# Kernel tuning notes

Hardware: AMD Instinct MI355X
Metric: run time of the kernel (lower is better)

Reference implementation:

```python
import jax, jax.numpy as jnp
import numpy as np

B, K, D, H = 16384, 3, 1024, 16
DH = D // H  # head_dim = 64


def setup_inputs() -> dict:
    key = jax.random.key(0)
    ks = jax.random.split(key, 12)
    s = 1.0 / np.sqrt(D)
    inp = {
        "tokens": jax.random.normal(ks[0], (B, K, D), dtype=jnp.float32),
        "ctx": jax.random.normal(ks[1], (B, 1, D), dtype=jnp.float32),
        "Wq": jax.random.uniform(ks[2], (D, D), jnp.float32, -s, s),
        "bq": jnp.zeros((D,), jnp.float32),
        "Wk": jax.random.uniform(ks[3], (D, D), jnp.float32, -s, s),
        "bk": jnp.zeros((D,), jnp.float32),
        "Wv": jax.random.uniform(ks[4], (D, D), jnp.float32, -s, s),
        "bv": jnp.zeros((D,), jnp.float32),
        "Wc": jax.random.uniform(ks[5], (D, D), jnp.float32, -s, s),
        "bc": jnp.zeros((D,), jnp.float32),
        "Wo": jax.random.uniform(ks[6], (D, D), jnp.float32, -s, s),
        "bo": jnp.zeros((D,), jnp.float32),
    }
    return inp


def _split_heads(x):
    # (B, L, D) -> (B, H, L, DH)
    Bq, L, _ = x.shape
    return x.reshape(Bq, L, H, DH).transpose(0, 2, 1, 3)


def reference(tokens, ctx, Wq, bq, Wk, bk, Wv, bv, Wc, bc, Wo, bo):
    q = _split_heads(tokens @ Wq.T + bq)          # (B,H,K,DH)
    k = _split_heads(tokens @ Wk.T + bk)          # (B,H,K,DH)
    v = _split_heads(tokens @ Wv.T + bv)          # (B,H,K,DH)
    c = _split_heads(ctx @ Wc.T + bc)             # (B,H,1,DH)
    k_ctx = k * c                                  # context-modulated keys
    v_ctx = v * c                                  # context-modulated values
    scores = jnp.einsum("bhqd,bhkd->bhqk", q, k_ctx) / jnp.sqrt(jnp.float32(DH))
    probs = jax.nn.softmax(scores, axis=-1)       # dropout p=0.0 -> identity
    out = jnp.einsum("bhqk,bhkd->bhqd", probs, v_ctx)
    out = out.transpose(0, 2, 1, 3).reshape(tokens.shape[0], K, D)  # merge heads
    return out @ Wo.T + bo
```

## Files before the change

kernel.cpp:

```cpp
#include <hip/hip_runtime.h>
#include <hip/hip_bf16.h>

#define BB 16384
#define KK 3
#define DD 1024
#define HH 16

typedef __attribute__((ext_vector_type(8))) short bf16x8;
typedef __attribute__((ext_vector_type(4))) float f32x4;
typedef unsigned int u32;

__device__ __forceinline__ void load_lds16(const void* g, void* l) {
  __builtin_amdgcn_global_load_lds(
      (const __attribute__((address_space(1))) u32*)g,
      (__attribute__((address_space(3))) u32*)l,
      16, 0, 0);
}

__device__ __forceinline__ unsigned short f2bf(float f) {
  __hip_bfloat16 h = __float2bfloat16(f);
  unsigned short u;
  __builtin_memcpy(&u, &h, 2);
  return u;
}

__device__ __forceinline__ float bf2f(unsigned short u) {
  union { float f; u32 i; } cv;
  cv.i = ((u32)u) << 16;
  return cv.f;
}

__global__ void cast_f32_bf16(const float* __restrict__ in,
                              unsigned short* __restrict__ out, int n4) {
  int stride = gridDim.x * blockDim.x;
  for (int i = blockIdx.x * blockDim.x + threadIdx.x; i < n4; i += stride) {
    float4 v = ((const float4*)in)[i];
    ushort4 o;
    o.x = f2bf(v.x);
    o.y = f2bf(v.y);
    o.z = f2bf(v.z);
    o.w = f2bf(v.w);
    ((ushort4*)out)[i] = o;
  }
}

template <bool OUT_F32>
__global__ __launch_bounds__(512, 2)
void gemm256(const __hip_bfloat16* __restrict__ A,
             const __hip_bfloat16* __restrict__ Bt,
             const float* __restrict__ bias,
             void* __restrict__ Cout,
             int M, int N, int K) {
  __shared__ __align__(128) char lds[131072];

  const int nTn = N >> 8;
  const int nwg = (M >> 8) * nTn;
  int bid = blockIdx.x;
  bid = (bid & 7) * (nwg >> 3) + (bid >> 3);
  const int tm = bid / nTn;
  const int tn = bid % nTn;

  const int tid = threadIdx.x;
  const int l = tid & 63;
  const int w = tid >> 6;
  const int wm = w >> 2;
  const int wn = w & 3;
  const int l15 = l & 15;
  const int g = l >> 4;
  const int l7 = l15 & 7;

  const int rA = l15 << 7;
  const int cs0 = ((g ^ l7) << 4);
  const int cs1 = (((4 | g) ^ l7) << 4);

  const size_t strideK = (size_t)K * 2;
  const char* Ab = (const char*)A + (size_t)tm * 256 * strideK;
  const char* Bb = (const char*)Bt + (size_t)tn * 256 * strideK;
  const int sld = tid << 4;
  const int lch = (((tid & 7) ^ ((tid >> 3) & 7)) << 4);
  const size_t so0 = (size_t)(tid >> 3) * strideK + lch;
  const size_t so1 = so0 + (size_t)64 * strideK;
  const size_t h1 = (size_t)128 * strideK;

  f32x4 acc[8][4] = {};
  const int nkt = K >> 6;

#define STAGE(T)                                                          \
  {                                                                       \
    char* bb = lds + (((T) & 1) << 16);                                   \
    const char* ga = Ab + ((size_t)(T) << 7);                             \
    const char* gb = Bb + ((size_t)(T) << 7);                             \
    load_lds16(ga + so0, bb + sld);                                       \
    load_lds16(ga + so1, bb + 8192 + sld);                                \
    load_lds16(ga + h1 + so0, bb + 16384 + sld);                          \
    load_lds16(ga + h1 + so1, bb + 16384 + 8192 + sld);                   \
    load_lds16(gb + so0, bb + 32768 + sld);                               \
    load_lds16(gb + so1, bb + 32768 + 8192 + sld);                        \
    load_lds16(gb + h1 + so0, bb + 49152 + sld);                          \
    load_lds16(gb + h1 + so1, bb + 49152 + 8192 + sld);                   \
  }

#define MFMA_BLK(M0)                                                      \
  __builtin_amdgcn_s_setprio(1);                                          \
  _Pragma("unroll") for (int mm = 0; mm < 4; ++mm)                        \
      _Pragma("unroll") for (int nn = 0; nn < 4; ++nn)                    \
          acc[(M0) + mm][nn] = __builtin_amdgcn_mfma_f32_16x16x32_bf16(   \
              af[(M0) + mm], bfr[nn], acc[(M0) + mm][nn], 0, 0, 0);       \
  __builtin_amdgcn_s_setprio(0);

  STAGE(0);
  STAGE(1);

  for (int kt = 0; kt < nkt; ++kt) {
    const char* Ah = lds + ((kt & 1) << 16) + (wm << 14);
    const char* Bh = lds + ((kt & 1) << 16) + 32768 + (wn << 13);

    if (kt < nkt - 1)
      asm volatile("s_waitcnt vmcnt(8)" ::: "memory");
    else
      asm volatile("s_waitcnt vmcnt(0)" ::: "memory");
    __builtin_amdgcn_s_barrier();
    asm volatile("" ::: "memory");

    bf16x8 af[8], bfr[4];
#pragma unroll
    for (int m = 0; m < 8; ++m)
      af[m] = *(const bf16x8*)(Ah + (m << 11) + rA + cs0);
#pragma unroll
    for (int n = 0; n < 4; ++n)
      bfr[n] = *(const bf16x8*)(Bh + (n << 11) + rA + cs0);

    MFMA_BLK(0)
    MFMA_BLK(4)

#pragma unroll
    for (int m = 0; m < 8; ++m)
      af[m] = *(const bf16x8*)(Ah + (m << 11) + rA + cs1);
#pragma unroll
    for (int n = 0; n < 4; ++n)
      bfr[n] = *(const bf16x8*)(Bh + (n << 11) + rA + cs1);

    MFMA_BLK(0)

    asm volatile("s_waitcnt lgkmcnt(0)" ::: "memory");
    __builtin_amdgcn_sched_barrier(0);
    __builtin_amdgcn_s_barrier();
    asm volatile("" ::: "memory");

    if (kt + 2 < nkt) STAGE(kt + 2);

    MFMA_BLK(4)
  }
#undef STAGE
#undef MFMA_BLK

  const int cbase = tn * 256 + (wn << 6) + l15;
  float b4[4];
#pragma unroll
  for (int n = 0; n < 4; ++n) b4[n] = bias[cbase + (n << 4)];
  const size_t rbase = (size_t)tm * 256 + (wm << 7) + ((l >> 4) << 2);
#pragma unroll
  for (int m = 0; m < 8; ++m) {
#pragma unroll
    for (int j = 0; j < 4; ++j) {
      const size_t row = rbase + (m << 4) + j;
#pragma unroll
      for (int n = 0; n < 4; ++n) {
        const int col = cbase + (n << 4);
        float v = acc[m][n][j] + b4[n];
        if (OUT_F32)
          ((float*)Cout)[row * N + col] = v;
        else
          ((unsigned short*)Cout)[row * N + col] = f2bf(v);
      }
    }
  }
}

__global__ __launch_bounds__(256)
void attn_kernel(const unsigned short* __restrict__ QKV,
                 const unsigned short* __restrict__ Cp,
                 unsigned short* __restrict__ Out) {
  const int t = threadIdx.x;
  const int grp = (blockIdx.x << 4) + (t >> 4);
  const int x = t & 15;
  const int b = grp >> 4;
  const int h = grp & 15;

  const size_t col = (size_t)h * 64 + (x << 2);
  const size_t qbase = (size_t)b * 3 * 3072 + col;

  ushort4 cu = *(const ushort4*)&Cp[(size_t)b * 1024 + col];
  float c[4] = {bf2f(cu.x), bf2f(cu.y), bf2f(cu.z), bf2f(cu.w)};

  float q[3][4], kc[3][4], vc[3][4];
#pragma unroll
  for (int i = 0; i < 3; ++i) {
    ushort4 qu = *(const ushort4*)&QKV[qbase + (size_t)i * 3072];
    ushort4 ku = *(const ushort4*)&QKV[qbase + (size_t)i * 3072 + 1024];
    ushort4 vu = *(const ushort4*)&QKV[qbase + (size_t)i * 3072 + 2048];
    q[i][0] = bf2f(qu.x); q[i][1] = bf2f(qu.y); q[i][2] = bf2f(qu.z); q[i][3] = bf2f(qu.w);
    kc[i][0] = bf2f(ku.x) * c[0]; kc[i][1] = bf2f(ku.y) * c[1];
    kc[i][2] = bf2f(ku.z) * c[2]; kc[i][3] = bf2f(ku.w) * c[3];
    vc[i][0] = bf2f(vu.x) * c[0]; vc[i][1] = bf2f(vu.y) * c[1];
    vc[i][2] = bf2f(vu.z) * c[2]; vc[i][3] = bf2f(vu.w) * c[3];
  }

  float s[9];
#pragma unroll
  for (int i = 0; i < 3; ++i)
#pragma unroll
    for (int j = 0; j < 3; ++j)
      s[i * 3 + j] = q[i][0] * kc[j][0] + q[i][1] * kc[j][1] +
                     q[i][2] * kc[j][2] + q[i][3] * kc[j][3];

#pragma unroll
  for (int off = 8; off > 0; off >>= 1)
#pragma unroll
    for (int e = 0; e < 9; ++e)
      s[e] += __shfl_xor(s[e], off, 64);

  const float scale = 0.125f;
#pragma unroll
  for (int i = 0; i < 3; ++i) {
    float s0 = s[i * 3 + 0] * scale;
    float s1 = s[i * 3 + 1] * scale;
    float s2 = s[i * 3 + 2] * scale;
    float m = fmaxf(fmaxf(s0, s1), s2);
    float p0 = expf(s0 - m), p1 = expf(s1 - m), p2 = expf(s2 - m);
    float inv = 1.0f / (p0 + p1 + p2);
    ushort4 o;
    o.x = f2bf((p0 * vc[0][0] + p1 * vc[1][0] + p2 * vc[2][0]) * inv);
    o.y = f2bf((p0 * vc[0][1] + p1 * vc[1][1] + p2 * vc[2][1]) * inv);
    o.z = f2bf((p0 * vc[0][2] + p1 * vc[1][2] + p2 * vc[2][2]) * inv);
    o.w = f2bf((p0 * vc[0][3] + p1 * vc[1][3] + p2 * vc[2][3]) * inv);
    *(ushort4*)&Out[(size_t)(b * 3 + i) * 1024 + col] = o;
  }
}

extern "C" void kernel_launch(void* const* d_in, const int* in_sizes, int n_in,
                              void* d_out, int out_size, void* d_ws, size_t ws_size,
                              hipStream_t stream) {
  const float* tokens = (const float*)d_in[0];
  const float* ctx    = (const float*)d_in[1];
  const float* Wq     = (const float*)d_in[2];
  const float* bq     = (const float*)d_in[3];
  const float* Wk     = (const float*)d_in[4];
  const float* bk     = (const float*)d_in[5];
  const float* Wv     = (const float*)d_in[6];
  const float* bv     = (const float*)d_in[7];
  const float* Wc     = (const float*)d_in[8];
  const float* bc     = (const float*)d_in[9];
  const float* Wo     = (const float*)d_in[10];
  const float* bo     = (const float*)d_in[11];

  const int M  = BB * KK;
  const int Mc = BB;
  const int D  = DD;

  char* p = (char*)d_ws;
  auto carve = [&](size_t bytes) {
    char* r = p;
    p += (bytes + 255) & ~(size_t)255;
    return r;
  };
  unsigned short* Xb   = (unsigned short*)carve((size_t)M * D * 2);
  unsigned short* Cin  = (unsigned short*)carve((size_t)Mc * D * 2);
  unsigned short* Wqkv = (unsigned short*)carve((size_t)3 * D * D * 2);
  unsigned short* Wcb  = (unsigned short*)carve((size_t)D * D * 2);
  unsigned short* Wob  = (unsigned short*)carve((size_t)D * D * 2);
  float*          bqkv = (float*)carve((size_t)3 * D * 4);
  unsigned short* QKV  = (unsigned short*)carve((size_t)M * 3 * D * 2);
  unsigned short* Cpr  = (unsigned short*)carve((size_t)Mc * D * 2);

  hipLaunchKernelGGL(cast_f32_bf16, dim3(4096), dim3(256), 0, stream, tokens, Xb, M * D / 4);
  hipLaunchKernelGGL(cast_f32_bf16, dim3(2048), dim3(256), 0, stream, ctx, Cin, Mc * D / 4);
  hipLaunchKernelGGL(cast_f32_bf16, dim3(512), dim3(256), 0, stream, Wq, Wqkv, D * D / 4);
  hipLaunchKernelGGL(cast_f32_bf16, dim3(512), dim3(256), 0, stream, Wk, Wqkv + D * D, D * D / 4);
  hipLaunchKernelGGL(cast_f32_bf16, dim3(512), dim3(256), 0, stream, Wv, Wqkv + 2 * D * D, D * D / 4);
  hipLaunchKernelGGL(cast_f32_bf16, dim3(512), dim3(256), 0, stream, Wc, Wcb, D * D / 4);
  hipLaunchKernelGGL(cast_f32_bf16, dim3(512), dim3(256), 0, stream, Wo, Wob, D * D / 4);
  hipMemcpyAsync(bqkv, bq, D * 4, hipMemcpyDeviceToDevice, stream);
  hipMemcpyAsync(bqkv + D, bk, D * 4, hipMemcpyDeviceToDevice, stream);
  hipMemcpyAsync(bqkv + 2 * D, bv, D * 4, hipMemcpyDeviceToDevice, stream);

  hipLaunchKernelGGL((gemm256<false>), dim3((M / 256) * (3 * D / 256)), dim3(512), 0, stream,
                     (const __hip_bfloat16*)Xb, (const __hip_bfloat16*)Wqkv, bqkv,
                     (void*)QKV, M, 3 * D, D);
  hipLaunchKernelGGL((gemm256<false>), dim3((Mc / 256) * (D / 256)), dim3(512), 0, stream,
                     (const __hip_bfloat16*)Cin, (const __hip_bfloat16*)Wcb, bc,
                     (void*)Cpr, Mc, D, D);
  hipLaunchKernelGGL(attn_kernel, dim3(BB * HH / 16), dim3(256), 0, stream, QKV, Cpr, Xb);
  hipLaunchKernelGGL((gemm256<true>), dim3((M / 256) * (D / 256)), dim3(512), 0, stream,
                     (const __hip_bfloat16*)Xb, (const __hip_bfloat16*)Wob, bo,
                     d_out, M, D, D);
}
```

Measured before the change: 679.3 us.

## Restructure GEMM mainloop into 4-slot K=32 pipeline with split A/B staging

Replaces the double-buffered K=64 mainloop with a four-slot ring of K=32 tiles, prefetching three tiles ahead and issuing A and B global-to-LDS loads separately between the two MFMA halves. LDS fragment addressing and the swizzle are recomputed for the new 32-wide tile layout, and register pressure drops because only 4 A fragments are held at once. The aim is deeper latency hiding of global loads behind MFMA work. In exchange it adds more barriers per K step and halves the MFMA work between synchronizations.

```diff
diff --git a/kernel.cpp b/kernel.cpp
--- a/kernel.cpp
+++ b/kernel.cpp
@@ -69,90 +69,83 @@
   const int g = l >> 4;
   const int l7 = l15 & 7;
 
-  const int rA = l15 << 7;
-  const int cs0 = ((g ^ l7) << 4);
-  const int cs1 = (((4 | g) ^ l7) << 4);
+  const int aBase = (l15 << 7) + (((wm << 2) + g) ^ l7) * 16;
+  const int bBase = 16384 + ((((wn & 1) << 6) + l15) << 7) +
+                    ((((wn >> 1) << 2) + g) ^ l7) * 16;
 
   const size_t strideK = (size_t)K * 2;
   const char* Ab = (const char*)A + (size_t)tm * 256 * strideK;
   const char* Bb = (const char*)Bt + (size_t)tn * 256 * strideK;
+  const int q = (tid & 7) ^ ((tid >> 3) & 7);
+  const size_t g0 = (size_t)((q >> 2) * 128 + (tid >> 3)) * strideK + (q & 3) * 16;
+  const size_t g1 = g0 + (size_t)64 * strideK;
   const int sld = tid << 4;
-  const int lch = (((tid & 7) ^ ((tid >> 3) & 7)) << 4);
-  const size_t so0 = (size_t)(tid >> 3) * strideK + lch;
-  const size_t so1 = so0 + (size_t)64 * strideK;
-  const size_t h1 = (size_t)128 * strideK;
 
   f32x4 acc[8][4] = {};
-  const int nkt = K >> 6;
-
-#define STAGE(T)                                                          \
+  const int nkt = K >> 5;
+
+#define STAGE_A(T)                                                        \
   {                                                                       \
-    char* bb = lds + (((T) & 1) << 16);                                   \
-    const char* ga = Ab + ((size_t)(T) << 7);                             \
-    const char* gb = Bb + ((size_t)(T) << 7);                             \
-    load_lds16(ga + so0, bb + sld);                                       \
-    load_lds16(ga + so1, bb + 8192 + sld);                                \
-    load_lds16(ga + h1 + so0, bb + 16384 + sld);                          \
-    load_lds16(ga + h1 + so1, bb + 16384 + 8192 + sld);                   \
-    load_lds16(gb + so0, bb + 32768 + sld);                               \
-    load_lds16(gb + so1, bb + 32768 + 8192 + sld);                        \
-    load_lds16(gb + h1 + so0, bb + 49152 + sld);                          \
-    load_lds16(gb + h1 + so1, bb + 49152 + 8192 + sld);                   \
-  }
-
-#define MFMA_BLK(M0)                                                      \
+    char* sb = lds + (((T) & 3) << 15);                                   \
+    const char* ga = Ab + ((size_t)(T) << 6);                             \
+    load_lds16(ga + g0, sb + sld);                                        \
+    load_lds16(ga + g1, sb + 8192 + sld);                                 \
+  }
+#define STAGE_B(T)                                                        \
+  {                                                                       \
+    char* sb = lds + (((T) & 3) << 15);                                   \
+    const char* gb = Bb + ((size_t)(T) << 6);                             \
+    load_lds16(gb + g0, sb + 16384 + sld);                                \
+    load_lds16(gb + g1, sb + 24576 + sld);                                \
+  }
+#define MFMA_HALF(H)                                                      \
   __builtin_amdgcn_s_setprio(1);                                          \
   _Pragma("unroll") for (int mm = 0; mm < 4; ++mm)                        \
       _Pragma("unroll") for (int nn = 0; nn < 4; ++nn)                    \
-          acc[(M0) + mm][nn] = __builtin_amdgcn_mfma_f32_16x16x32_bf16(   \
-              af[(M0) + mm], bfr[nn], acc[(M0) + mm][nn], 0, 0, 0);       \
+          acc[(H) + mm][nn] = __builtin_amdgcn_mfma_f32_16x16x32_bf16(    \
+              af[mm], bfr[nn], acc[(H) + mm][nn], 0, 0, 0);               \
   __builtin_amdgcn_s_setprio(0);
 
-  STAGE(0);
-  STAGE(1);
+  STAGE_A(0); STAGE_B(0);
+  STAGE_A(1); STAGE_B(1);
+  STAGE_A(2); STAGE_B(2);
+  asm volatile("s_waitcnt vmcnt(8)" ::: "memory");
+  __builtin_amdgcn_s_barrier();
 
   for (int kt = 0; kt < nkt; ++kt) {
-    const char* Ah = lds + ((kt & 1) << 16) + (wm << 14);
-    const char* Bh = lds + ((kt & 1) << 16) + 32768 + (wn << 13);
-
-    if (kt < nkt - 1)
+    const char* slot = lds + ((kt & 3) << 15);
+    bf16x8 af[4], bfr[4];
+
+#pragma unroll
+    for (int n = 0; n < 4; ++n)
+      bfr[n] = *(const bf16x8*)(slot + bBase + (n << 11));
+#pragma unroll
+    for (int m = 0; m < 4; ++m)
+      af[m] = *(const bf16x8*)(slot + aBase + (m << 11));
+    if (kt + 3 < nkt) STAGE_A(kt + 3);
+    __builtin_amdgcn_s_barrier();
+    asm volatile("s_waitcnt lgkmcnt(0)" ::: "memory");
+    MFMA_HALF(0)
+    __builtin_amdgcn_s_barrier();
+
+#pragma unroll
+    for (int m = 0; m < 4; ++m)
+      af[m] = *(const bf16x8*)(slot + aBase + ((m + 4) << 11));
+    if (kt + 3 < nkt) STAGE_B(kt + 3);
+    if (kt < nkt - 3)
       asm volatile("s_waitcnt vmcnt(8)" ::: "memory");
-    else
+    else if (kt == nkt - 3)
+      asm volatile("s_waitcnt vmcnt(4)" ::: "memory");
+    else if (kt == nkt - 2)
       asm volatile("s_waitcnt vmcnt(0)" ::: "memory");
     __builtin_amdgcn_s_barrier();
-    asm volatile("" ::: "memory");
-
-    bf16x8 af[8], bfr[4];
-#pragma unroll
-    for (int m = 0; m < 8; ++m)
-      af[m] = *(const bf16x8*)(Ah + (m << 11) + rA + cs0);
-#pragma unroll
-    for (int n = 0; n < 4; ++n)
-      bfr[n] = *(const bf16x8*)(Bh + (n << 11) + rA + cs0);
-
-    MFMA_BLK(0)
-    MFMA_BLK(4)
-
-#pragma unroll
-    for (int m = 0; m < 8; ++m)
-      af[m] = *(const bf16x8*)(Ah + (m << 11) + rA + cs1);
-#pragma unroll
-    for (int n = 0; n < 4; ++n)
-      bfr[n] = *(const bf16x8*)(Bh + (n << 11) + rA + cs1);
-
-    MFMA_BLK(0)
-
     asm volatile("s_waitcnt lgkmcnt(0)" ::: "memory");
-    __builtin_amdgcn_sched_barrier(0);
-    __builtin_amdgcn_s_barrier();
-    asm volatile("" ::: "memory");
-
-    if (kt + 2 < nkt) STAGE(kt + 2);
-
-    MFMA_BLK(4)
-  }
-#undef STAGE
-#undef MFMA_BLK
+    MFMA_HALF(4)
+    __builtin_amdgcn_s_barrier();
+  }
+#undef STAGE_A
+#undef STAGE_B
+#undef MFMA_HALF
 
   const int cbase = tn * 256 + (wn << 6) + l15;
   float b4[4];
```

Result: no change. 666.4 us (-1.9%).
